# Performance work log

Measured on AMD Instinct MI355X. Metric: run time of the kernel, lower is better.

## Reference

```python
import jax, jax.numpy as jnp
import numpy as np

N = 50000
E = 800000
IN_DIM = 256
HID = 64
HEADS = 4
OUT_DIM = 40
NEG_SLOPE = 0.2


def _gatv2_conv(x, src, dst, Wl, bl, Wr, br, att, bias, concat):
    """PyG GATv2Conv (share_weights=False, eval mode, no attn dropout).
    src -> message source nodes, dst -> target nodes (softmax over dst)."""
    H, C = att.shape
    n = x.shape[0]
    xl = (x @ Wl + bl).reshape(n, H, C)  # source/message transform (lin_l)
    xr = (x @ Wr + br).reshape(n, H, C)  # target transform (lin_r)
    # per-edge logits: [E, H]
    s = xl[src] + xr[dst]                                  # [E,H,C]
    e = jnp.einsum('ehc,hc->eh', jax.nn.leaky_relu(s, NEG_SLOPE), att)
    # segment softmax over incoming edges of each target node
    m = jax.ops.segment_max(e, dst, num_segments=n)        # [N,H]
    m = jnp.where(jnp.isfinite(m), m, 0.0)                 # empty segments
    ex = jnp.exp(e - m[dst])
    denom = jax.ops.segment_sum(ex, dst, num_segments=n)   # [N,H]
    alpha = ex / (denom[dst] + 1e-16)                      # [E,H]
    out = jax.ops.segment_sum(alpha[:, :, None] * xl[src], dst, num_segments=n)
    if concat:
        out = out.reshape(n, H * C)
    else:
        out = out.mean(axis=1)
    return out + bias


def setup_inputs() -> dict:
    key = jax.random.key(0)
    ks = jax.random.split(key, 12)
    sc = 0.05
    return {
        'x': jax.random.normal(ks[0], (N, IN_DIM), jnp.float32),
        'src': jax.random.randint(ks[1], (E,), 0, N, jnp.int32),
        'dst': jax.random.randint(ks[2], (E,), 0, N, jnp.int32),
        'Wl1': jax.random.normal(ks[3], (IN_DIM, HEADS * HID), jnp.float32) * sc,
        'bl1': jnp.zeros((HEADS * HID,), jnp.float32),
        'Wr1': jax.random.normal(ks[4], (IN_DIM, HEADS * HID), jnp.float32) * sc,
        'br1': jnp.zeros((HEADS * HID,), jnp.float32),
        'att1': jax.random.normal(ks[5], (HEADS, HID), jnp.float32) * sc,
        'bias1': jnp.zeros((HEADS * HID,), jnp.float32),
        'Wl2': jax.random.normal(ks[6], (HEADS * HID, HEADS * HID), jnp.float32) * sc,
        'bl2': jnp.zeros((HEADS * HID,), jnp.float32),
        'Wr2': jax.random.normal(ks[7], (HEADS * HID, HEADS * HID), jnp.float32) * sc,
        'br2': jnp.zeros((HEADS * HID,), jnp.float32),
        'att2': jax.random.normal(ks[8], (HEADS, HID), jnp.float32) * sc,
        'bias2': jnp.zeros((HID,), jnp.float32),
        'Wc': jax.random.normal(ks[9], (HID, OUT_DIM), jnp.float32) * sc,
        'bc': jnp.zeros((OUT_DIM,), jnp.float32),
    }


def reference(x, src, dst, Wl1, bl1, Wr1, br1, att1, bias1,
              Wl2, bl2, Wr2, br2, att2, bias2, Wc, bc):
    h = _gatv2_conv(x, src, dst, Wl1, bl1, Wr1, br1, att1, bias1, concat=True)
    h = jax.nn.relu(h)  # dropout p applied only in training; eval -> identity
    h = _gatv2_conv(h, src, dst, Wl2, bl2, Wr2, br2, att2, bias2, concat=False)
    h = jax.nn.relu(h)
    return h @ Wc + bc  # [N, OUT_DIM]
```

## Files before the change

### kernel.cpp

```cpp
#include <hip/hip_runtime.h>
#include <hip/hip_bf16.h>
#include <math.h>


#define IN_DIM 256
#define HIDHC 256
#define HID 64
#define OUT_DIM 40

using half8  = __attribute__((ext_vector_type(8))) _Float16;
using half4  = __attribute__((ext_vector_type(4))) _Float16;
using half2v = __attribute__((ext_vector_type(2))) _Float16;
using f32x4  = __attribute__((ext_vector_type(4))) float;

__device__ __forceinline__ void gload16(const void* g, void* l) {
    __builtin_amdgcn_global_load_lds(
        (const __attribute__((address_space(1))) void*)g,
        (__attribute__((address_space(3))) void*)l, 16, 0, 0);
}


__global__ void edge_hist(const int* __restrict__ dst, int* __restrict__ deg, int E) {
    int i = blockIdx.x * blockDim.x + threadIdx.x;
    if (i < E) atomicAdd(&deg[dst[i]], 1);
}

__global__ void deg_block_reduce(const int* __restrict__ deg, int* __restrict__ bsum, int n) {
    int i = blockIdx.x * 256 + threadIdx.x;
    int v = (i < n) ? deg[i] : 0;
    #pragma unroll
    for (int off = 32; off; off >>= 1) v += __shfl_xor(v, off, 64);
    __shared__ int ws[4];
    int lane = threadIdx.x & 63, wid = threadIdx.x >> 6;
    if (lane == 0) ws[wid] = v;
    __syncthreads();
    if (threadIdx.x == 0) bsum[blockIdx.x] = ws[0] + ws[1] + ws[2] + ws[3];
}

__global__ void scan_bsums(const int* __restrict__ bsum, int* __restrict__ bpre, int nb) {
    __shared__ int s[256];
    int tid = threadIdx.x;
    int orig = (tid < nb) ? bsum[tid] : 0;
    s[tid] = orig;
    __syncthreads();
    #pragma unroll
    for (int off = 1; off < 256; off <<= 1) {
        int t = (tid >= off) ? s[tid - off] : 0;
        __syncthreads();
        s[tid] += t;
        __syncthreads();
    }
    if (tid < nb) bpre[tid] = s[tid] - orig;
}

__global__ void deg_scan_apply(const int* __restrict__ deg, const int* __restrict__ bpre,
                               int* __restrict__ offsets, int* __restrict__ cursor, int n) {
    int i = blockIdx.x * 256 + threadIdx.x;
    int lane = threadIdx.x & 63, wid = threadIdx.x >> 6;
    int v = (i < n) ? deg[i] : 0;
    int inc = v;
    #pragma unroll
    for (int off = 1; off < 64; off <<= 1) {
        int t = __shfl_up(inc, off, 64);
        if (lane >= off) inc += t;
    }
    __shared__ int ws[4];
    if (lane == 63) ws[wid] = inc;
    __syncthreads();
    int add = bpre[blockIdx.x];
    for (int w = 0; w < wid; ++w) add += ws[w];
    int incl = inc + add;
    if (i < n) { offsets[i + 1] = incl; cursor[i] = incl - v; }
    if (i == 0) offsets[0] = 0;
}

__global__ void edge_scatter(const int* __restrict__ src, const int* __restrict__ dst,
                             int* __restrict__ cursor, int* __restrict__ csr_src, int E) {
    int i = blockIdx.x * blockDim.x + threadIdx.x;
    if (i < E) {
        int p = atomicAdd(&cursor[dst[i]], 1);
        csr_src[p] = src[i];
    }
}


__global__ void prep_inputs(const float* __restrict__ x, _Float16* __restrict__ Af,
                            const float* __restrict__ W0, const float* __restrict__ W1,
                            const float* __restrict__ W2, const float* __restrict__ W3,
                            _Float16* __restrict__ T, int n4, int nb_cvt) {
    if ((int)blockIdx.x < nb_cvt) {
        int i = blockIdx.x * blockDim.x + threadIdx.x;
        if (i >= n4) return;
        float4 v = ((const float4*)x)[i];
        half4 h = { (_Float16)v.x, (_Float16)v.y, (_Float16)v.z, (_Float16)v.w };
        int node = i >> 6;
        int kb = (i & 63) * 4;
        size_t a = (size_t)(node >> 7) * 32768 + (size_t)(kb >> 3) * 1024
                 + (size_t)(node & 127) * 8 + (kb & 7);
        *(half4*)(Af + a) = h;
    } else {
        int widx = blockIdx.x - nb_cvt;
        int wsel = widx >> 8, k = widx & 255, nn = threadIdx.x;
        const float* Wsel = (wsel == 0) ? W0 : (wsel == 1) ? W1
                          : (wsel == 2) ? W2 : W3;
        float v = Wsel[k * 256 + nn];
        size_t a = (size_t)wsel * 65536
                 + (size_t)(nn >> 7) * 32768 + (size_t)(k >> 5) * 4096
                 + (size_t)((k >> 3) & 3) * 1024 + (size_t)(nn & 127) * 8 + (k & 7);
        T[a] = (_Float16)v;
    }
}


__global__ __launch_bounds__(512) void gemm_dual(
    const _Float16* __restrict__ Apk,
    const _Float16* __restrict__ W0, const float* __restrict__ b0, _Float16* __restrict__ C0,
    const _Float16* __restrict__ W1, const float* __restrict__ b1, _Float16* __restrict__ C1,
    int M)
{
    __shared__ __align__(16) _Float16 sA[2][4096];
    __shared__ __align__(16) _Float16 sW[2][2][4096];

    int tid = threadIdx.x;
    int bm = blockIdx.x * 128;
    int bn = blockIdx.y * 128;

    int lane = tid & 63, w = tid >> 6;
    int z  = w >> 2, wq = w & 3;
    int r = lane & 15, q = lane >> 4;
    int m0 = (wq >> 1) * 64, n0 = (wq & 1) * 64;

    const _Float16* Abase = Apk + (size_t)blockIdx.x * 32768;
    const _Float16* W0b   = W0  + (size_t)blockIdx.y * 32768;
    const _Float16* W1b   = W1  + (size_t)blockIdx.y * 32768;
    int go = tid * 8;

    f32x4 acc[4][4];
    #pragma unroll
    for (int i = 0; i < 4; ++i)
        #pragma unroll
        for (int j = 0; j < 4; ++j) acc[i][j] = (f32x4)0.f;

    gload16(Abase + go, &sA[0][go]);
    gload16(W0b + go, &sW[0][0][go]);
    gload16(W1b + go, &sW[0][1][go]);
    __builtin_amdgcn_s_waitcnt(0);
    __syncthreads();

    #pragma unroll 1
    for (int kt = 0; kt < 8; ++kt) {
        int buf = kt & 1;
        if (kt < 7) {
            int k0 = (kt + 1) * 4096;
            gload16(Abase + k0 + go, &sA[buf ^ 1][go]);
            gload16(W0b + k0 + go, &sW[buf ^ 1][0][go]);
            gload16(W1b + k0 + go, &sW[buf ^ 1][1][go]);
        }
        half8 a[4], b[4];
        #pragma unroll
        for (int i = 0; i < 4; ++i) {
            a[i] = *(const half8*)(&sA[buf][(q * 128 + m0 + i * 16 + r) * 8]);
            b[i] = *(const half8*)(&sW[buf][z][(q * 128 + n0 + i * 16 + r) * 8]);
        }
        #pragma unroll
        for (int i = 0; i < 4; ++i)
            #pragma unroll
            for (int j = 0; j < 4; ++j)
                acc[i][j] = __builtin_amdgcn_mfma_f32_16x16x32_f16(a[i], b[j], acc[i][j], 0, 0, 0);
        __builtin_amdgcn_s_waitcnt(0);
        __syncthreads();
    }

    const float* bias = z ? b1 : b0;
    _Float16*    C    = z ? C1 : C0;

    float bv[4];
    #pragma unroll
    for (int j = 0; j < 4; ++j) bv[j] = bias[bn + n0 + j * 16 + r];
    #pragma unroll
    for (int i = 0; i < 4; ++i) {
        #pragma unroll
        for (int reg = 0; reg < 4; ++reg) {
            int orow = bm + m0 + i * 16 + q * 4 + reg;
            if (orow < M) {
                #pragma unroll
                for (int j = 0; j < 4; ++j)
                    C[(size_t)orow * 256 + bn + n0 + j * 16 + r] =
                        (_Float16)(acc[i][j][reg] + bv[j]);
            }
        }
    }
}


__global__ __launch_bounds__(256) void gat_node(
    const _Float16* __restrict__ xl, const _Float16* __restrict__ xr,
    const float* __restrict__ att, const float* __restrict__ bias,
    const int* __restrict__ offsets, const int* __restrict__ csr_src,
    void* __restrict__ out0, int n, int mode)
{
    int wid = threadIdx.x >> 6;
    int node = (blockIdx.x << 2) + wid;
    if (node >= n) return;
    int lane = threadIdx.x & 63;
    int H = lane >> 5;
    int p = lane & 31;

    const half2v c02 = { (_Float16)0.2f, (_Float16)0.2f };

    half8 xrh = *(const half8*)(xr + (size_t)node * HIDHC + p * 8);
    half2v xr01 = __builtin_shufflevector(xrh, xrh, 0, 1);
    half2v xr23 = __builtin_shufflevector(xrh, xrh, 2, 3);
    half2v xr45 = __builtin_shufflevector(xrh, xrh, 4, 5);
    half2v xr67 = __builtin_shufflevector(xrh, xrh, 6, 7);

    float4 af0 = *(const float4*)(att + p * 8);
    float4 af1 = *(const float4*)(att + p * 8 + 4);
    half2v at01 = { (_Float16)af0.x, (_Float16)af0.y };
    half2v at23 = { (_Float16)af0.z, (_Float16)af0.w };
    half2v at45 = { (_Float16)af1.x, (_Float16)af1.y };
    half2v at67 = { (_Float16)af1.z, (_Float16)af1.w };

    float acc[8];
    #pragma unroll
    for (int k = 0; k < 8; ++k) acc[k] = 0.f;
    float d = 0.f;

    auto edge_compute = [&](half8 h) {
        half2v h01 = __builtin_shufflevector(h, h, 0, 1);
        half2v h23 = __builtin_shufflevector(h, h, 2, 3);
        half2v h45 = __builtin_shufflevector(h, h, 4, 5);
        half2v h67 = __builtin_shufflevector(h, h, 6, 7);
        half2v s01 = h01 + xr01, s23 = h23 + xr23, s45 = h45 + xr45, s67 = h67 + xr67;
        half2v l01 = __builtin_elementwise_max(s01, s01 * c02);
        half2v l23 = __builtin_elementwise_max(s23, s23 * c02);
        half2v l45 = __builtin_elementwise_max(s45, s45 * c02);
        half2v l67 = __builtin_elementwise_max(s67, s67 * c02);
        float e = __builtin_amdgcn_fdot2(l01, at01, 0.f, false);
        e = __builtin_amdgcn_fdot2(l23, at23, e, false);
        e = __builtin_amdgcn_fdot2(l45, at45, e, false);
        e = __builtin_amdgcn_fdot2(l67, at67, e, false);
        e += __shfl_xor(e, 1);
        e += __shfl_xor(e, 2);
        e += __shfl_xor(e, 4);
        float pw = __expf(e);
        d += pw;
        #pragma unroll
        for (int k = 0; k < 8; ++k) acc[k] = fmaf(pw, (float)h[k], acc[k]);
    };

    int j0 = __builtin_amdgcn_readfirstlane(offsets[node]);
    int j1 = __builtin_amdgcn_readfirstlane(offsets[node + 1]);
    int deg = j1 - j0;

    int fast = min(deg, 64);
    int npf = fast >> 1;
    int idxv = 0;
    if (lane < fast) idxv = csr_src[j0 + lane];

    half8 hA, hB;
    if (npf > 0) { int s = __shfl(idxv, 0 + H, 64); hA = *(const half8*)(xl + (size_t)s * HIDHC + p * 8); }
    if (npf > 1) { int s = __shfl(idxv, 2 + H, 64); hB = *(const half8*)(xl + (size_t)s * HIDHC + p * 8); }
    int t = 0;
    for (; t + 4 <= npf; t += 2) {
        half8 ha = hA, hb = hB;
        { int s = __shfl(idxv, (t + 2) * 2 + H, 64); hA = *(const half8*)(xl + (size_t)s * HIDHC + p * 8); }
        { int s = __shfl(idxv, (t + 3) * 2 + H, 64); hB = *(const half8*)(xl + (size_t)s * HIDHC + p * 8); }
        edge_compute(ha);
        edge_compute(hb);
    }
    if (t + 2 <= npf) {
        half8 ha = hA, hb = hB;
        if (t + 2 < npf) { int s = __shfl(idxv, (t + 2) * 2 + H, 64); hA = *(const half8*)(xl + (size_t)s * HIDHC + p * 8); }
        edge_compute(ha);
        edge_compute(hb);
        t += 2;
    }
    if (t < npf) {
        edge_compute(hA);
    }

    int j = j0 + (npf << 1);
    for (; j + 2 <= j1; j += 2) {
        int s0 = __builtin_amdgcn_readfirstlane(csr_src[j]);
        int s1 = __builtin_amdgcn_readfirstlane(csr_src[j + 1]);
        int s = H ? s1 : s0;
        half8 h = *(const half8*)(xl + (size_t)s * HIDHC + p * 8);
        edge_compute(h);
    }
    if (j < j1) {
        int s0 = __builtin_amdgcn_readfirstlane(csr_src[j]);
        half8 h = *(const half8*)(xl + (size_t)s0 * HIDHC + p * 8);
        half2v h01 = __builtin_shufflevector(h, h, 0, 1);
        half2v h23 = __builtin_shufflevector(h, h, 2, 3);
        half2v h45 = __builtin_shufflevector(h, h, 4, 5);
        half2v h67 = __builtin_shufflevector(h, h, 6, 7);
        half2v s01 = h01 + xr01, s23 = h23 + xr23, s45 = h45 + xr45, s67 = h67 + xr67;
        half2v l01 = __builtin_elementwise_max(s01, s01 * c02);
        half2v l23 = __builtin_elementwise_max(s23, s23 * c02);
        half2v l45 = __builtin_elementwise_max(s45, s45 * c02);
        half2v l67 = __builtin_elementwise_max(s67, s67 * c02);
        float e = __builtin_amdgcn_fdot2(l01, at01, 0.f, false);
        e = __builtin_amdgcn_fdot2(l23, at23, e, false);
        e = __builtin_amdgcn_fdot2(l45, at45, e, false);
        e = __builtin_amdgcn_fdot2(l67, at67, e, false);
        e += __shfl_xor(e, 1);
        e += __shfl_xor(e, 2);
        e += __shfl_xor(e, 4);
        float pw = (H == 0) ? __expf(e) : 0.f;
        d += pw;
        #pragma unroll
        for (int k = 0; k < 8; ++k) acc[k] = fmaf(pw, (float)h[k], acc[k]);
    }

    d += __shfl_xor(d, 32);
    #pragma unroll
    for (int k = 0; k < 8; ++k) acc[k] += __shfl_xor(acc[k], 32);

    float inv = 1.f / (d + 1e-16f);
    float o[8];
    #pragma unroll
    for (int k = 0; k < 8; ++k) o[k] = acc[k] * inv;

    if (mode == 0) {
        if (H == 0) {
            float4 b0 = *(const float4*)(bias + p * 8);
            float4 b1 = *(const float4*)(bias + p * 8 + 4);
            float bb[8] = { b0.x, b0.y, b0.z, b0.w, b1.x, b1.y, b1.z, b1.w };
            half8 hh;
            #pragma unroll
            for (int k = 0; k < 8; ++k) hh[k] = (_Float16)fmaxf(o[k] + bb[k], 0.f);
            _Float16* dst = (_Float16*)out0 + (size_t)(node >> 7) * 32768
                          + (size_t)p * 1024 + (size_t)(node & 127) * 8;
            *(half8*)dst = hh;
        }
    } else {
        #pragma unroll
        for (int k = 0; k < 8; ++k) {
            o[k] += __shfl_xor(o[k], 8);
            o[k] += __shfl_xor(o[k], 16);
        }
        if (lane < 8) {
            float4 b0 = *(const float4*)(bias + p * 8);
            float4 b1 = *(const float4*)(bias + p * 8 + 4);
            float bb[8] = { b0.x, b0.y, b0.z, b0.w, b1.x, b1.y, b1.z, b1.w };
            float4 o0, o1;
            o0.x = fmaxf(o[0] * 0.25f + bb[0], 0.f);
            o0.y = fmaxf(o[1] * 0.25f + bb[1], 0.f);
            o0.z = fmaxf(o[2] * 0.25f + bb[2], 0.f);
            o0.w = fmaxf(o[3] * 0.25f + bb[3], 0.f);
            o1.x = fmaxf(o[4] * 0.25f + bb[4], 0.f);
            o1.y = fmaxf(o[5] * 0.25f + bb[5], 0.f);
            o1.z = fmaxf(o[6] * 0.25f + bb[6], 0.f);
            o1.w = fmaxf(o[7] * 0.25f + bb[7], 0.f);
            float* dst = (float*)out0 + (size_t)node * HID + p * 8;
            *(float4*)dst = o0;
            *(float4*)(dst + 4) = o1;
        }
    }
}


__global__ __launch_bounds__(256) void final_linear(
    const float* __restrict__ h2, const float* __restrict__ Wc,
    const float* __restrict__ bc, float* __restrict__ out, int n)
{
    __shared__ float Ws[HID * OUT_DIM];
    __shared__ float bs[OUT_DIM];
    __shared__ float hs[64][HID + 1];

    for (int i = threadIdx.x; i < HID * OUT_DIM; i += 256) Ws[i] = Wc[i];
    if (threadIdx.x < OUT_DIM) bs[threadIdx.x] = bc[threadIdx.x];

    int n0 = blockIdx.x * 64;
    for (int i = threadIdx.x; i < 64 * HID; i += 256) {
        int r = i >> 6, c = i & 63;
        int node = n0 + r;
        hs[r][c] = (node < n) ? h2[(size_t)node * HID + c] : 0.f;
    }
    __syncthreads();

    for (int idx = threadIdx.x; idx < 64 * OUT_DIM; idx += 256) {
        int r = idx / OUT_DIM, o = idx % OUT_DIM;
        int node = n0 + r;
        if (node < n) {
            float s = bs[o];
            #pragma unroll
            for (int c = 0; c < HID; ++c) s = fmaf(hs[r][c], Ws[c * OUT_DIM + o], s);
            out[(size_t)node * OUT_DIM + o] = s;
        }
    }
}


extern "C" void kernel_launch(void* const* d_in, const int* in_sizes, int n_in,
                              void* d_out, int out_size, void* d_ws, size_t ws_size,
                              hipStream_t stream) {
    const int N = in_sizes[0] / IN_DIM;
    const int E = in_sizes[1];

    const float* x    = (const float*)d_in[0];
    const int*   src  = (const int*)d_in[1];
    const int*   dst  = (const int*)d_in[2];
    const float* Wl1  = (const float*)d_in[3];
    const float* bl1  = (const float*)d_in[4];
    const float* Wr1  = (const float*)d_in[5];
    const float* br1  = (const float*)d_in[6];
    const float* att1 = (const float*)d_in[7];
    const float* bias1= (const float*)d_in[8];
    const float* Wl2  = (const float*)d_in[9];
    const float* bl2  = (const float*)d_in[10];
    const float* Wr2  = (const float*)d_in[11];
    const float* br2  = (const float*)d_in[12];
    const float* att2 = (const float*)d_in[13];
    const float* bias2= (const float*)d_in[14];
    const float* Wc   = (const float*)d_in[15];
    const float* bc   = (const float*)d_in[16];

    char* ws = (char*)d_ws;
    size_t off = 0;
    const int NT = (N + 127) / 128;
    _Float16* xlh = (_Float16*)(ws + off); off += (size_t)N * HIDHC * 2;
    _Float16* xrh = (_Float16*)(ws + off); off += (size_t)N * HIDHC * 2;
    _Float16* Af  = (_Float16*)(ws + off); off += (size_t)NT * 32768 * 2;
    float*    h2  = (float*)(ws + off);    off += (size_t)N * HID * 4;
    _Float16* Wt  = (_Float16*)(ws + off); off += (size_t)4 * 65536 * 2;
    int* deg     = (int*)(ws + off); off += (size_t)N * 4;
    int* offsets = (int*)(ws + off); off += (size_t)(N + 1) * 4;
    int* cursor  = (int*)(ws + off); off += (size_t)N * 4;
    int* csr     = (int*)(ws + off); off += (size_t)E * 4;
    int* bsum    = (int*)(ws + off); off += 256 * 4;
    int* bpre    = (int*)(ws + off); off += 256 * 4;

    const int NB = (N + 255) / 256;

    hipMemsetAsync(deg, 0, (size_t)N * 4, stream);
    if (N & 127)
        hipMemsetAsync(Af + (size_t)(NT - 1) * 32768, 0, 32768 * 2, stream);
    edge_hist<<<(E + 255) / 256, 256, 0, stream>>>(dst, deg, E);
    deg_block_reduce<<<NB, 256, 0, stream>>>(deg, bsum, N);
    scan_bsums<<<1, 256, 0, stream>>>(bsum, bpre, NB);
    deg_scan_apply<<<NB, 256, 0, stream>>>(deg, bpre, offsets, cursor, N);
    edge_scatter<<<(E + 255) / 256, 256, 0, stream>>>(src, dst, cursor, csr, E);
    const int n4 = N * HIDHC / 4;
    const int nb_cvt = (n4 + 255) / 256;
    prep_inputs<<<nb_cvt + 1024, 256, 0, stream>>>(x, Af, Wl1, Wr1, Wl2, Wr2,
                                                   Wt, n4, nb_cvt);

    const int KW = 65536;
    dim3 gg(NT, 2);
    gemm_dual<<<gg, 512, 0, stream>>>(Af,
        Wt + 0 * KW, bl1, xlh,
        Wt + 1 * KW, br1, xrh, N);
    gat_node<<<(N + 3) / 4, 256, 0, stream>>>(xlh, xrh, att1, bias1, offsets, csr,
                                              (void*)Af, N, 0);
    gemm_dual<<<gg, 512, 0, stream>>>(Af,
        Wt + 2 * KW, bl2, xlh,
        Wt + 3 * KW, br2, xrh, N);
    gat_node<<<(N + 3) / 4, 256, 0, stream>>>(xlh, xrh, att2, bias2, offsets, csr,
                                              (void*)h2, N, 1);
    final_linear<<<(N + 63) / 64, 256, 0, stream>>>(h2, Wc, bc, (float*)d_out, N);
}
```

Before: 435.5 us.

## Merge preprocessing launches: fuse histogram with input prep and scatter with GEMM

Folds the degree histogram into the input/weight conversion kernel and merges the block-prefix scan into deg_scan_apply, which removes the single-block scan_bsums launch. It also runs the CSR edge scatter as extra blocks of the first dual GEMM launch. The goal is fewer kernel launches and serial gaps, and letting the atomic scatter overlap with the GEMM tiles. The cost is that each scan block now re-reduces every preceding block sum, and blocks of very different kinds share one grid.

```diff
diff --git a/kernel.cpp b/kernel.cpp
--- a/kernel.cpp
+++ b/kernel.cpp
@@ -20,76 +20,18 @@
 }
 
 
-__global__ void edge_hist(const int* __restrict__ dst, int* __restrict__ deg, int E) {
-    int i = blockIdx.x * blockDim.x + threadIdx.x;
-    if (i < E) atomicAdd(&deg[dst[i]], 1);
-}
-
-__global__ void deg_block_reduce(const int* __restrict__ deg, int* __restrict__ bsum, int n) {
-    int i = blockIdx.x * 256 + threadIdx.x;
-    int v = (i < n) ? deg[i] : 0;
-    #pragma unroll
-    for (int off = 32; off; off >>= 1) v += __shfl_xor(v, off, 64);
-    __shared__ int ws[4];
-    int lane = threadIdx.x & 63, wid = threadIdx.x >> 6;
-    if (lane == 0) ws[wid] = v;
-    __syncthreads();
-    if (threadIdx.x == 0) bsum[blockIdx.x] = ws[0] + ws[1] + ws[2] + ws[3];
-}
-
-__global__ void scan_bsums(const int* __restrict__ bsum, int* __restrict__ bpre, int nb) {
-    __shared__ int s[256];
-    int tid = threadIdx.x;
-    int orig = (tid < nb) ? bsum[tid] : 0;
-    s[tid] = orig;
-    __syncthreads();
-    #pragma unroll
-    for (int off = 1; off < 256; off <<= 1) {
-        int t = (tid >= off) ? s[tid - off] : 0;
-        __syncthreads();
-        s[tid] += t;
-        __syncthreads();
-    }
-    if (tid < nb) bpre[tid] = s[tid] - orig;
-}
-
-__global__ void deg_scan_apply(const int* __restrict__ deg, const int* __restrict__ bpre,
-                               int* __restrict__ offsets, int* __restrict__ cursor, int n) {
-    int i = blockIdx.x * 256 + threadIdx.x;
-    int lane = threadIdx.x & 63, wid = threadIdx.x >> 6;
-    int v = (i < n) ? deg[i] : 0;
-    int inc = v;
-    #pragma unroll
-    for (int off = 1; off < 64; off <<= 1) {
-        int t = __shfl_up(inc, off, 64);
-        if (lane >= off) inc += t;
-    }
-    __shared__ int ws[4];
-    if (lane == 63) ws[wid] = inc;
-    __syncthreads();
-    int add = bpre[blockIdx.x];
-    for (int w = 0; w < wid; ++w) add += ws[w];
-    int incl = inc + add;
-    if (i < n) { offsets[i + 1] = incl; cursor[i] = incl - v; }
-    if (i == 0) offsets[0] = 0;
-}
-
-__global__ void edge_scatter(const int* __restrict__ src, const int* __restrict__ dst,
-                             int* __restrict__ cursor, int* __restrict__ csr_src, int E) {
-    int i = blockIdx.x * blockDim.x + threadIdx.x;
-    if (i < E) {
-        int p = atomicAdd(&cursor[dst[i]], 1);
-        csr_src[p] = src[i];
-    }
-}
-
-
-__global__ void prep_inputs(const float* __restrict__ x, _Float16* __restrict__ Af,
-                            const float* __restrict__ W0, const float* __restrict__ W1,
-                            const float* __restrict__ W2, const float* __restrict__ W3,
-                            _Float16* __restrict__ T, int n4, int nb_cvt) {
-    if ((int)blockIdx.x < nb_cvt) {
-        int i = blockIdx.x * blockDim.x + threadIdx.x;
+__global__ void hist_prep(const int* __restrict__ dst, int* __restrict__ deg,
+                          int E, int nbh,
+                          const float* __restrict__ x, _Float16* __restrict__ Af,
+                          const float* __restrict__ W0, const float* __restrict__ W1,
+                          const float* __restrict__ W2, const float* __restrict__ W3,
+                          _Float16* __restrict__ T, int n4, int nb_cvt) {
+    int bid = blockIdx.x;
+    if (bid < nbh) {
+        int i = bid * 256 + threadIdx.x;
+        if (i < E) atomicAdd(&deg[dst[i]], 1);
+    } else if (bid < nbh + nb_cvt) {
+        int i = (bid - nbh) * 256 + threadIdx.x;
         if (i >= n4) return;
         float4 v = ((const float4*)x)[i];
         half4 h = { (_Float16)v.x, (_Float16)v.y, (_Float16)v.z, (_Float16)v.w };
@@ -99,7 +41,7 @@
                  + (size_t)(node & 127) * 8 + (kb & 7);
         *(half4*)(Af + a) = h;
     } else {
-        int widx = blockIdx.x - nb_cvt;
+        int widx = bid - nbh - nb_cvt;
         int wsel = widx >> 8, k = widx & 255, nn = threadIdx.x;
         const float* Wsel = (wsel == 0) ? W0 : (wsel == 1) ? W1
                           : (wsel == 2) ? W2 : W3;
@@ -111,28 +53,71 @@
     }
 }
 
-
-__global__ __launch_bounds__(512) void gemm_dual(
+__global__ void deg_block_reduce(const int* __restrict__ deg, int* __restrict__ bsum, int n) {
+    int i = blockIdx.x * 256 + threadIdx.x;
+    int v = (i < n) ? deg[i] : 0;
+    #pragma unroll
+    for (int off = 32; off; off >>= 1) v += __shfl_xor(v, off, 64);
+    __shared__ int ws[4];
+    int lane = threadIdx.x & 63, wid = threadIdx.x >> 6;
+    if (lane == 0) ws[wid] = v;
+    __syncthreads();
+    if (threadIdx.x == 0) bsum[blockIdx.x] = ws[0] + ws[1] + ws[2] + ws[3];
+}
+
+__global__ void deg_scan_apply(const int* __restrict__ deg, const int* __restrict__ bsum,
+                               int* __restrict__ offsets, int* __restrict__ cursor,
+                               int n, int nb) {
+    int tid = threadIdx.x;
+    int lane = tid & 63, wid = tid >> 6;
+
+    __shared__ int pws[4];
+    __shared__ int sadd;
+    int pv = (tid < nb && tid < (int)blockIdx.x) ? bsum[tid] : 0;
+    #pragma unroll
+    for (int off = 32; off; off >>= 1) pv += __shfl_xor(pv, off, 64);
+    if (lane == 0) pws[wid] = pv;
+    __syncthreads();
+    if (tid == 0) sadd = pws[0] + pws[1] + pws[2] + pws[3];
+    __syncthreads();
+
+    int i = blockIdx.x * 256 + tid;
+    int v = (i < n) ? deg[i] : 0;
+    int inc = v;
+    #pragma unroll
+    for (int off = 1; off < 64; off <<= 1) {
+        int t = __shfl_up(inc, off, 64);
+        if (lane >= off) inc += t;
+    }
+    __shared__ int ws[4];
+    if (lane == 63) ws[wid] = inc;
+    __syncthreads();
+    int add = sadd;
+    for (int w = 0; w < wid; ++w) add += ws[w];
+    int incl = inc + add;
+    if (i < n) { offsets[i + 1] = incl; cursor[i] = incl - v; }
+    if (i == 0) offsets[0] = 0;
+}
+
+
+__device__ __forceinline__ void gemm_tile(
     const _Float16* __restrict__ Apk,
     const _Float16* __restrict__ W0, const float* __restrict__ b0, _Float16* __restrict__ C0,
     const _Float16* __restrict__ W1, const float* __restrict__ b1, _Float16* __restrict__ C1,
-    int M)
+    int M, int bx, int by, _Float16* sA, _Float16* sW)
 {
-    __shared__ __align__(16) _Float16 sA[2][4096];
-    __shared__ __align__(16) _Float16 sW[2][2][4096];
-
     int tid = threadIdx.x;
-    int bm = blockIdx.x * 128;
-    int bn = blockIdx.y * 128;
+    int bm = bx * 128;
+    int bn = by * 128;
 
     int lane = tid & 63, w = tid >> 6;
     int z  = w >> 2, wq = w & 3;
     int r = lane & 15, q = lane >> 4;
     int m0 = (wq >> 1) * 64, n0 = (wq & 1) * 64;
 
-    const _Float16* Abase = Apk + (size_t)blockIdx.x * 32768;
-    const _Float16* W0b   = W0  + (size_t)blockIdx.y * 32768;
-    const _Float16* W1b   = W1  + (size_t)blockIdx.y * 32768;
+    const _Float16* Abase = Apk + (size_t)bx * 32768;
+    const _Float16* W0b   = W0  + (size_t)by * 32768;
+    const _Float16* W1b   = W1  + (size_t)by * 32768;
     int go = tid * 8;
 
     f32x4 acc[4][4];
@@ -141,9 +126,9 @@
         #pragma unroll
         for (int j = 0; j < 4; ++j) acc[i][j] = (f32x4)0.f;
 
-    gload16(Abase + go, &sA[0][go]);
-    gload16(W0b + go, &sW[0][0][go]);
-    gload16(W1b + go, &sW[0][1][go]);
+    gload16(Abase + go, sA + go);
+    gload16(W0b + go, sW + go);
+    gload16(W1b + go, sW + 4096 + go);
     __builtin_amdgcn_s_waitcnt(0);
     __syncthreads();
 
@@ -152,15 +137,15 @@
         int buf = kt & 1;
         if (kt < 7) {
             int k0 = (kt + 1) * 4096;
-            gload16(Abase + k0 + go, &sA[buf ^ 1][go]);
-            gload16(W0b + k0 + go, &sW[buf ^ 1][0][go]);
-            gload16(W1b + k0 + go, &sW[buf ^ 1][1][go]);
+            gload16(Abase + k0 + go, sA + (buf ^ 1) * 4096 + go);
+            gload16(W0b + k0 + go, sW + ((buf ^ 1) * 2 + 0) * 4096 + go);
+            gload16(W1b + k0 + go, sW + ((buf ^ 1) * 2 + 1) * 4096 + go);
         }
         half8 a[4], b[4];
         #pragma unroll
         for (int i = 0; i < 4; ++i) {
-            a[i] = *(const half8*)(&sA[buf][(q * 128 + m0 + i * 16 + r) * 8]);
-            b[i] = *(const half8*)(&sW[buf][z][(q * 128 + n0 + i * 16 + r) * 8]);
+            a[i] = *(const half8*)(sA + buf * 4096 + (q * 128 + m0 + i * 16 + r) * 8);
+            b[i] = *(const half8*)(sW + (buf * 2 + z) * 4096 + (q * 128 + n0 + i * 16 + r) * 8);
         }
         #pragma unroll
         for (int i = 0; i < 4; ++i)
@@ -190,6 +175,39 @@
             }
         }
     }
+}
+
+__global__ __launch_bounds__(512) void gemm_dual(
+    const _Float16* __restrict__ Apk,
+    const _Float16* __restrict__ W0, const float* __restrict__ b0, _Float16* __restrict__ C0,
+    const _Float16* __restrict__ W1, const float* __restrict__ b1, _Float16* __restrict__ C1,
+    int M)
+{
+    __shared__ __align__(16) _Float16 sA[2 * 4096];
+    __shared__ __align__(16) _Float16 sW[2 * 2 * 4096];
+    gemm_tile(Apk, W0, b0, C0, W1, b1, C1, M, blockIdx.x, blockIdx.y, sA, sW);
+}
+
+__global__ __launch_bounds__(512) void gemm_scatter(
+    const _Float16* __restrict__ Apk,
+    const _Float16* __restrict__ W0, const float* __restrict__ b0, _Float16* __restrict__ C0,
+    const _Float16* __restrict__ W1, const float* __restrict__ b1, _Float16* __restrict__ C1,
+    int M, int nbs,
+    const int* __restrict__ src, const int* __restrict__ dst,
+    int* __restrict__ cursor, int* __restrict__ csr_src, int E)
+{
+    __shared__ __align__(16) _Float16 sA[2 * 4096];
+    __shared__ __align__(16) _Float16 sW[2 * 2 * 4096];
+    if ((int)blockIdx.x < nbs) {
+        int e = blockIdx.x * 512 + threadIdx.x;
+        if (e < E) {
+            int p = atomicAdd(&cursor[dst[e]], 1);
+            csr_src[p] = src[e];
+        }
+        return;
+    }
+    int g = blockIdx.x - nbs;
+    gemm_tile(Apk, W0, b0, C0, W1, b1, C1, M, g >> 1, g & 1, sA, sW);
 }
 
 
@@ -430,31 +448,32 @@
     int* cursor  = (int*)(ws + off); off += (size_t)N * 4;
     int* csr     = (int*)(ws + off); off += (size_t)E * 4;
     int* bsum    = (int*)(ws + off); off += 256 * 4;
-    int* bpre    = (int*)(ws + off); off += 256 * 4;
 
     const int NB = (N + 255) / 256;
 
     hipMemsetAsync(deg, 0, (size_t)N * 4, stream);
     if (N & 127)
         hipMemsetAsync(Af + (size_t)(NT - 1) * 32768, 0, 32768 * 2, stream);
-    edge_hist<<<(E + 255) / 256, 256, 0, stream>>>(dst, deg, E);
-    deg_block_reduce<<<NB, 256, 0, stream>>>(deg, bsum, N);
-    scan_bsums<<<1, 256, 0, stream>>>(bsum, bpre, NB);
-    deg_scan_apply<<<NB, 256, 0, stream>>>(deg, bpre, offsets, cursor, N);
-    edge_scatter<<<(E + 255) / 256, 256, 0, stream>>>(src, dst, cursor, csr, E);
+
+    const int nbh = (E + 255) / 256;
     const int n4 = N * HIDHC / 4;
     const int nb_cvt = (n4 + 255) / 256;
-    prep_inputs<<<nb_cvt + 1024, 256, 0, stream>>>(x, Af, Wl1, Wr1, Wl2, Wr2,
-                                                   Wt, n4, nb_cvt);
+    hist_prep<<<nbh + nb_cvt + 1024, 256, 0, stream>>>(
+        dst, deg, E, nbh, x, Af, Wl1, Wr1, Wl2, Wr2, Wt, n4, nb_cvt);
+
+    deg_block_reduce<<<NB, 256, 0, stream>>>(deg, bsum, N);
+    deg_scan_apply<<<NB, 256, 0, stream>>>(deg, bsum, offsets, cursor, N, NB);
 
     const int KW = 65536;
-    dim3 gg(NT, 2);
-    gemm_dual<<<gg, 512, 0, stream>>>(Af,
+    const int nbs = (E + 511) / 512;
+    gemm_scatter<<<nbs + 2 * NT, 512, 0, stream>>>(Af,
         Wt + 0 * KW, bl1, xlh,
-        Wt + 1 * KW, br1, xrh, N);
+        Wt + 1 * KW, br1, xrh, N, nbs,
+        src, dst, cursor, csr, E);
+
     gat_node<<<(N + 3) / 4, 256, 0, stream>>>(xlh, xrh, att1, bias1, offsets, csr,
                                               (void*)Af, N, 0);
-    gemm_dual<<<gg, 512, 0, stream>>>(Af,
+    gemm_dual<<<dim3(NT, 2), 512, 0, stream>>>(Af,
         Wt + 2 * KW, bl2, xlh,
         Wt + 3 * KW, br2, xrh, N);
     gat_node<<<(N + 3) / 4, 256, 0, stream>>>(xlh, xrh, att2, bias2, offsets, csr,
```

Measured after the change: 415.5 us. 4.6% less time.
